# Optimization experiments

Measured on AMD Instinct MI355X. Metric: run time of the kernel, lower is better.

## Reference

```python
import jax, jax.numpy as jnp
import numpy as np

BETA = 0.25


def setup_inputs() -> dict:
    key = jax.random.key(0)
    kx, ke = jax.random.split(key)
    x = jax.random.normal(kx, (32, 32, 32, 256), dtype=jnp.float32)
    embedding = jax.random.normal(ke, (256, 4096), dtype=jnp.float32) * 0.02
    return {"x": x, "embedding": embedding}


def reference(x, embedding):
    # x: [B, H, W, D]; embedding (codebook): [D, K]
    D = embedding.shape[0]
    flat = x.reshape(-1, D)                               # [N, D]
    sim = flat @ embedding                                # [N, K]
    dist = (jnp.sum(flat * flat, axis=1, keepdims=True)
            + jnp.sum(embedding * embedding, axis=0)
            - 2.0 * sim)                                  # [N, K]
    idx = jnp.argmin(dist, axis=1)                        # [N]
    # one-hot @ embedding.T  ==  gather rows of embedding.T
    quantized = jnp.take(embedding.T, idx, axis=0).reshape(x.shape)
    commitment_loss = BETA * jnp.mean((jax.lax.stop_gradient(quantized) - x) ** 2)
    codebook_loss = jnp.mean((quantized - jax.lax.stop_gradient(x)) ** 2)
    loss = commitment_loss + codebook_loss
    # straight-through estimator
    quantized_st = x + jax.lax.stop_gradient(quantized - x)
    return quantized_st, loss
```

## Files before the change

kernel.cpp:

```cpp
#include <hip/hip_runtime.h>
#include <math.h>

typedef _Float16 f16;
typedef f16 f16x8 __attribute__((ext_vector_type(8)));
typedef float f32x4 __attribute__((ext_vector_type(4)));

#define N_ROWS 32768
#define DIM    256
#define KCODES 4096

#define WS_ET    0
#define WS_BN    (WS_ET + KCODES*DIM)
#define WS_AN    (WS_BN + KCODES)
#define WS_PART  (WS_AN + N_ROWS)
#define WS_IDX   (WS_PART + 8192)
#define WS_BP    (WS_IDX + N_ROWS)
#define WS_AP    (WS_BP + 1048576)


__device__ __forceinline__ void gload16(const void* g, void* l) {
#if __has_builtin(__builtin_amdgcn_global_load_lds)
    __builtin_amdgcn_global_load_lds(
        (const __attribute__((address_space(1))) unsigned int*)g,
        (__attribute__((address_space(3))) unsigned int*)l, 16, 0, 0);
#else
    *(float4*)l = *(const float4*)g;
#endif
}

__global__ void vq_rownorm(const float* __restrict__ src, float* __restrict__ out, int nrows) {
    int w    = threadIdx.x >> 6;
    int lane = threadIdx.x & 63;
    int row  = blockIdx.x * 4 + w;
    if (row >= nrows) return;
    float4 v = *(const float4*)&src[row * DIM + lane * 4];
    float  s = v.x * v.x + v.y * v.y + v.z * v.z + v.w * v.w;
#pragma unroll
    for (int m = 1; m < 64; m <<= 1) s += __shfl_xor(s, m);
    if (lane == 0) out[row] = s;
}

__global__ void vq_prep_a(const float* __restrict__ x, char* __restrict__ Ap,
                          float* __restrict__ An) {
    const int t = threadIdx.x;
    const int lane = t & 63, w = t >> 6;
    const size_t row0 = (size_t)blockIdx.x * 128;
    char* base = Ap + (size_t)blockIdx.x * 131072;
    const int chunk = lane >> 4;
    const int dd2   = (lane & 15) * 8;
#pragma unroll 4
    for (int it = 0; it < 32; ++it) {
        const int m = it * 4 + w;
        float4 v = *(const float4*)&x[(row0 + m) * DIM + lane * 4];
        float vs[4] = { v.x, v.y, v.z, v.w };
        uint32_t hw[2], lw[2];
#pragma unroll
        for (int p = 0; p < 2; ++p) {
            uint32_t hword = 0, lword = 0;
#pragma unroll
            for (int j = 0; j < 2; ++j) {
                float s = vs[p * 2 + j] * 1024.0f;
                f16 h = (f16)s;
                f16 l = (f16)(s - (float)h);
                hword |= (uint32_t)__builtin_bit_cast(uint16_t, h) << (16 * j);
                lword |= (uint32_t)__builtin_bit_cast(uint16_t, l) << (16 * j);
            }
            hw[p] = hword; lw[p] = lword;
        }
        const int off = chunk * 16384 + m * 128 + (dd2 ^ ((m & 7) << 4));
        *(uint2*)(base + off)         = *(uint2*)hw;
        *(uint2*)(base + 65536 + off) = *(uint2*)lw;
        float s = v.x * v.x + v.y * v.y + v.z * v.z + v.w * v.w;
#pragma unroll
        for (int mm = 1; mm < 64; mm <<= 1) s += __shfl_xor(s, mm);
        if (lane == 0) An[row0 + m] = s;
    }
}

__global__ void vq_prep_b(const float* __restrict__ e, char* __restrict__ Bp,
                          float* __restrict__ et) {
    __shared__ float lt[128][65];
    const int t  = threadIdx.x;
    const int jb = blockIdx.x >> 2;
    const int c  = blockIdx.x & 3;
    const int d0 = c * 64, n0 = jb * 128;
#pragma unroll
    for (int it = 0; it < 8; ++it) {
        int linear = it * 256 + t;
        int drow = linear >> 5;
        int ncol = (linear & 31) * 4;
        float4 v = *(const float4*)&e[(size_t)(d0 + drow) * KCODES + n0 + ncol];
        lt[ncol + 0][drow] = v.x;
        lt[ncol + 1][drow] = v.y;
        lt[ncol + 2][drow] = v.z;
        lt[ncol + 3][drow] = v.w;
    }
    __syncthreads();
#pragma unroll
    for (int it = 0; it < 8; ++it) {
        int lin = it * 256 + t;
        int n = lin >> 4, q = lin & 15;
        float4 v = { lt[n][q*4], lt[n][q*4+1], lt[n][q*4+2], lt[n][q*4+3] };
        *(float4*)&et[(size_t)(n0 + n) * DIM + d0 + q * 4] = v;
    }
    char* ehbase = Bp + (size_t)jb * 131072 + c * 16384;
    const int n_loc = t >> 1;
    const int shalf = t & 1;
#pragma unroll
    for (int g = 0; g < 4; ++g) {
        const int dd8 = shalf * 32 + g * 8;
        uint32_t ehw[4], elw[4];
#pragma unroll
        for (int p = 0; p < 4; ++p) {
            uint32_t hword = 0, lword = 0;
#pragma unroll
            for (int j = 0; j < 2; ++j) {
                float s = lt[n_loc][dd8 + p * 2 + j] * 1024.0f;
                f16 h = (f16)s;
                f16 l = (f16)(s - (float)h);
                hword |= (uint32_t)__builtin_bit_cast(uint16_t, h) << (16 * j);
                lword |= (uint32_t)__builtin_bit_cast(uint16_t, l) << (16 * j);
            }
            ehw[p] = hword; elw[p] = lword;
        }
        const int off = n_loc * 128 + ((dd8 * 2) ^ ((n_loc & 7) << 4));
        *(uint4*)(ehbase + off)         = *(uint4*)ehw;
        *(uint4*)(ehbase + 65536 + off) = *(uint4*)elw;
    }
}

__global__ __launch_bounds__(512, 2) void vq_main(
    const char* __restrict__ Ap, const char* __restrict__ Bp,
    const float* __restrict__ An, const float* __restrict__ Bn,
    int* __restrict__ idxOut)
{
    __shared__ __align__(16) char LaH[2][16384];
    __shared__ __align__(16) char LaL[16384];
    __shared__ __align__(16) char LbEH[32768];
    __shared__ __align__(16) char LbEL[32768];
    __shared__ unsigned long long red[128][4];

    const int tid = threadIdx.x;
    const int wid = tid >> 6, lane = tid & 63;
    const int wr = wid >> 2, wc = wid & 3;
    const int hi = lane >> 4, ln = lane & 15;
    const int sx = (lane & 7) << 4;
    const size_t row0 = (size_t)blockIdx.x * 128;
    const char* abase = Ap + (size_t)blockIdx.x * 131072;

    float an[16];
#pragma unroll
    for (int mi = 0; mi < 4; ++mi)
#pragma unroll
        for (int r = 0; r < 4; ++r)
            an[mi * 4 + r] = An[row0 + wr * 64 + mi * 16 + hi * 4 + r];

    unsigned long long run[16];
#pragma unroll
    for (int v = 0; v < 16; ++v) run[v] = ~0ull;

#define ISSUE_Y(t)                                                           \
    do {                                                                     \
        const int tn = ((t) + 1) & 63;                                       \
        const int c_ = tn & 3, it_ = tn >> 2;                                \
        const char* b0_ = Bp + (size_t)(2 * it_) * 131072;                   \
        const char* b1_ = b0_ + 131072;                                      \
        char* ah_ = (char*)LaH[tn & 1];                                      \
        gload16(abase + c_ * 16384 + tid * 16,        ah_ + tid * 16);       \
        gload16(abase + c_ * 16384 + 8192 + tid * 16, ah_ + 8192 + tid * 16);\
        gload16(b0_ + c_ * 16384 + tid * 16,        LbEH + tid * 16);        \
        gload16(b0_ + c_ * 16384 + 8192 + tid * 16, LbEH + 8192 + tid * 16); \
        gload16(b1_ + c_ * 16384 + tid * 16,        LbEH + 16384 + tid * 16);\
        gload16(b1_ + c_ * 16384 + 8192 + tid * 16, LbEH + 24576 + tid * 16);\
        gload16(b0_ + 65536 + c_ * 16384 + tid * 16,        LbEL + tid * 16);\
        gload16(b0_ + 65536 + c_ * 16384 + 8192 + tid * 16, LbEL + 8192 + tid * 16);\
        gload16(b1_ + 65536 + c_ * 16384 + tid * 16,        LbEL + 16384 + tid * 16);\
        gload16(b1_ + 65536 + c_ * 16384 + 8192 + tid * 16, LbEL + 24576 + tid * 16);\
    } while (0)

#define ISSUE_X(t)                                                           \
    do {                                                                     \
        const int c_ = (t) & 3;                                              \
        gload16(abase + 65536 + c_ * 16384 + tid * 16,        LaL + tid * 16);\
        gload16(abase + 65536 + c_ * 16384 + 8192 + tid * 16, LaL + 8192 + tid * 16);\
    } while (0)

    f32x4 acc[4][4] = {};

    ISSUE_Y(63);

#pragma unroll 1
    for (int t = 0; t < 64; ++t) {
        ISSUE_X(t);
        asm volatile("s_waitcnt vmcnt(2)" ::: "memory");
        __builtin_amdgcn_s_barrier();
        __builtin_amdgcn_sched_barrier(0);

        const char* ah = LaH[t & 1];
        f16x8 aH[8], bH[8], bL[8];
#pragma unroll
        for (int ks = 0; ks < 2; ++ks) {
            const int ko = (ks * 64 + hi * 16) ^ sx;
#pragma unroll
            for (int i = 0; i < 4; ++i)
                aH[ks * 4 + i] = *(const f16x8*)(ah + (wr * 64 + i * 16 + ln) * 128 + ko);
#pragma unroll
            for (int ni = 0; ni < 4; ++ni) {
                const int brow = ((wc & 1) * 64 + ni * 16 + ln) * 128 + ko;
                bH[ks * 4 + ni] = *(const f16x8*)(LbEH + (wc >> 1) * 16384 + brow);
                bL[ks * 4 + ni] = *(const f16x8*)(LbEL + (wc >> 1) * 16384 + brow);
            }
        }
        __builtin_amdgcn_s_setprio(1);
#pragma unroll
        for (int ks = 0; ks < 2; ++ks)
#pragma unroll
            for (int mi = 0; mi < 4; ++mi)
#pragma unroll
                for (int ni = 0; ni < 4; ++ni)
                    acc[mi][ni] = __builtin_amdgcn_mfma_f32_16x16x32_f16(
                        aH[ks * 4 + mi], bH[ks * 4 + ni], acc[mi][ni], 0, 0, 0);
#pragma unroll
        for (int ks = 0; ks < 2; ++ks)
#pragma unroll
            for (int mi = 0; mi < 4; ++mi)
#pragma unroll
                for (int ni = 0; ni < 4; ++ni)
                    acc[mi][ni] = __builtin_amdgcn_mfma_f32_16x16x32_f16(
                        aH[ks * 4 + mi], bL[ks * 4 + ni], acc[mi][ni], 0, 0, 0);
        __builtin_amdgcn_s_setprio(0);
        __builtin_amdgcn_s_barrier();

        ISSUE_Y(t);
        asm volatile("s_waitcnt vmcnt(10)" ::: "memory");
        __builtin_amdgcn_s_barrier();
        __builtin_amdgcn_sched_barrier(0);

        f16x8 aL[8];
#pragma unroll
        for (int ks = 0; ks < 2; ++ks) {
            const int ko = (ks * 64 + hi * 16) ^ sx;
#pragma unroll
            for (int i = 0; i < 4; ++i)
                aL[ks * 4 + i] = *(const f16x8*)(LaL + (wr * 64 + i * 16 + ln) * 128 + ko);
        }
        __builtin_amdgcn_s_setprio(1);
#pragma unroll
        for (int ks = 0; ks < 2; ++ks)
#pragma unroll
            for (int mi = 0; mi < 4; ++mi)
#pragma unroll
                for (int ni = 0; ni < 4; ++ni)
                    acc[mi][ni] = __builtin_amdgcn_mfma_f32_16x16x32_f16(
                        aL[ks * 4 + mi], bH[ks * 4 + ni], acc[mi][ni], 0, 0, 0);
        __builtin_amdgcn_s_setprio(0);
        __builtin_amdgcn_s_barrier();

        if ((t & 3) == 3) {
            const int it = t >> 2;
            float bn[4];
#pragma unroll
            for (int ni = 0; ni < 4; ++ni)
                bn[ni] = Bn[it * 256 + wc * 64 + ni * 16 + ln];
#pragma unroll
            for (int mi = 0; mi < 4; ++mi)
#pragma unroll
                for (int r = 0; r < 4; ++r) {
                    const float a = an[mi * 4 + r];
                    unsigned long long best = run[mi * 4 + r];
#pragma unroll
                    for (int ni = 0; ni < 4; ++ni) {
                        float sim  = acc[mi][ni][r] * 0x1p-20f;
                        float tt   = a + bn[ni];
                        float dist = tt - 2.0f * sim;
                        unsigned code = (unsigned)(it * 256 + wc * 64 + ni * 16 + ln);
                        unsigned long long p =
                            ((unsigned long long)__float_as_uint(dist) << 32) | code;
                        best = p < best ? p : best;
                    }
                    run[mi * 4 + r] = best;
                }
#pragma unroll
            for (int mi = 0; mi < 4; ++mi)
#pragma unroll
                for (int ni = 0; ni < 4; ++ni)
                    acc[mi][ni] = f32x4{0.f, 0.f, 0.f, 0.f};
        }
    }
#undef ISSUE_X
#undef ISSUE_Y

#pragma unroll
    for (int v = 0; v < 16; ++v) {
#pragma unroll
        for (int m = 1; m < 16; m <<= 1) {
            unsigned long long o = __shfl_xor(run[v], m);
            run[v] = o < run[v] ? o : run[v];
        }
    }
    if (ln == 0) {
#pragma unroll
        for (int mi = 0; mi < 4; ++mi)
#pragma unroll
            for (int r = 0; r < 4; ++r)
                red[wr * 64 + mi * 16 + hi * 4 + r][wc] = run[mi * 4 + r];
    }
    __syncthreads();
    if (tid < 128) {
        unsigned long long b = red[tid][0];
#pragma unroll
        for (int w = 1; w < 4; ++w) {
            unsigned long long o = red[tid][w];
            b = o < b ? o : b;
        }
        idxOut[row0 + tid] = (int)(unsigned)(b & 0xffffffffull);
    }
}

__global__ void vq_gather(const float* __restrict__ x, const float* __restrict__ et,
                          const int* __restrict__ idx,
                          float* __restrict__ out, float* __restrict__ part) {
    __shared__ float wsum[4];
    int w    = threadIdx.x >> 6;
    int lane = threadIdx.x & 63;
    int row  = blockIdx.x * 4 + w;
    int k    = idx[row];
    float4 q  = *(const float4*)&et[(size_t)k * DIM + lane * 4];
    float4 xv = *(const float4*)&x[(size_t)row * DIM + lane * 4];
    *(float4*)&out[(size_t)row * DIM + lane * 4] = q;
    float d0 = q.x - xv.x, d1 = q.y - xv.y, d2 = q.z - xv.z, d3 = q.w - xv.w;
    float s = d0 * d0 + d1 * d1 + d2 * d2 + d3 * d3;
#pragma unroll
    for (int m = 1; m < 64; m <<= 1) s += __shfl_xor(s, m);
    if (lane == 0) wsum[w] = s;
    __syncthreads();
    if (threadIdx.x == 0) part[blockIdx.x] = wsum[0] + wsum[1] + wsum[2] + wsum[3];
}

__global__ void vq_finalize(const float* __restrict__ part, float* __restrict__ lossOut) {
    __shared__ float sm[256];
    float s = 0.0f;
    for (int i = threadIdx.x; i < 8192; i += 256) s += part[i];
    sm[threadIdx.x] = s;
    __syncthreads();
    for (int st = 128; st > 0; st >>= 1) {
        if (threadIdx.x < st) sm[threadIdx.x] += sm[threadIdx.x + st];
        __syncthreads();
    }
    if (threadIdx.x == 0)
        lossOut[0] = 1.25f * (sm[0] / 8388608.0f);
}

extern "C" void kernel_launch(void* const* d_in, const int* in_sizes, int n_in,
                              void* d_out, int out_size, void* d_ws, size_t ws_size,
                              hipStream_t stream) {
    const float* x = (const float*)d_in[0];
    const float* e = (const float*)d_in[1];
    float* out = (float*)d_out;
    float* ws  = (float*)d_ws;

    float* et   = ws + WS_ET;
    float* bn   = ws + WS_BN;
    float* an   = ws + WS_AN;
    float* part = ws + WS_PART;
    int*   idx  = (int*)(ws + WS_IDX);
    char*  Bp   = (char*)(ws + WS_BP);
    char*  Ap   = (char*)(ws + WS_AP);

    vq_prep_a<<<256, 256, 0, stream>>>(x, Ap, an);
    vq_prep_b<<<128, 256, 0, stream>>>(e, Bp, et);
    vq_rownorm<<<KCODES / 4, 256, 0, stream>>>(et, bn, KCODES);
    vq_main<<<256, 512, 0, stream>>>(Ap, Bp, an, bn, idx);
    vq_gather<<<N_ROWS / 4, 256, 0, stream>>>(x, et, idx, out, part);
    vq_finalize<<<1, 256, 0, stream>>>(part, out + (size_t)N_ROWS * DIM);
}
```

Baseline: 284.8 us.

## Restructure load pipeline to issue all next-step tiles after fragment reads

Merges the two staged global-to-LDS load groups into one issue per step, placed after all shared-memory fragment reads complete. The A-low tile becomes the double-buffered one instead of A-high, and the loop is unrolled by four with plain block barriers replacing explicit vmcnt waits. This simplifies synchronisation and lets all next-step loads overlap the full MFMA phase. The cost is that every step now waits for all outstanding loads at its top barrier.

```diff
diff --git a/kernel.cpp b/kernel.cpp
--- a/kernel.cpp
+++ b/kernel.cpp
@@ -134,8 +134,8 @@
     const float* __restrict__ An, const float* __restrict__ Bn,
     int* __restrict__ idxOut)
 {
-    __shared__ __align__(16) char LaH[2][16384];
-    __shared__ __align__(16) char LaL[16384];
+    __shared__ __align__(16) char LaH[16384];
+    __shared__ __align__(16) char LaL[2][16384];
     __shared__ __align__(16) char LbEH[32768];
     __shared__ __align__(16) char LbEL[32768];
     __shared__ unsigned long long red[128][4];
@@ -159,136 +159,135 @@
 #pragma unroll
     for (int v = 0; v < 16; ++v) run[v] = ~0ull;
 
-#define ISSUE_Y(t)                                                           \
-    do {                                                                     \
-        const int tn = ((t) + 1) & 63;                                       \
-        const int c_ = tn & 3, it_ = tn >> 2;                                \
-        const char* b0_ = Bp + (size_t)(2 * it_) * 131072;                   \
-        const char* b1_ = b0_ + 131072;                                      \
-        char* ah_ = (char*)LaH[tn & 1];                                      \
-        gload16(abase + c_ * 16384 + tid * 16,        ah_ + tid * 16);       \
-        gload16(abase + c_ * 16384 + 8192 + tid * 16, ah_ + 8192 + tid * 16);\
-        gload16(b0_ + c_ * 16384 + tid * 16,        LbEH + tid * 16);        \
-        gload16(b0_ + c_ * 16384 + 8192 + tid * 16, LbEH + 8192 + tid * 16); \
-        gload16(b1_ + c_ * 16384 + tid * 16,        LbEH + 16384 + tid * 16);\
-        gload16(b1_ + c_ * 16384 + 8192 + tid * 16, LbEH + 24576 + tid * 16);\
-        gload16(b0_ + 65536 + c_ * 16384 + tid * 16,        LbEL + tid * 16);\
-        gload16(b0_ + 65536 + c_ * 16384 + 8192 + tid * 16, LbEL + 8192 + tid * 16);\
-        gload16(b1_ + 65536 + c_ * 16384 + tid * 16,        LbEL + 16384 + tid * 16);\
-        gload16(b1_ + 65536 + c_ * 16384 + 8192 + tid * 16, LbEL + 24576 + tid * 16);\
+#define ISSUE(c_, it_, slot)                                                  \
+    do {                                                                      \
+        const char* b0_ = Bp + (size_t)(2 * (it_)) * 131072;                  \
+        const char* b1_ = b0_ + 131072;                                       \
+        gload16(abase + (c_) * 16384 + tid * 16,        LaH + tid * 16);      \
+        gload16(abase + (c_) * 16384 + 8192 + tid * 16, LaH + 8192 + tid * 16);\
+        gload16(abase + 65536 + (c_) * 16384 + tid * 16,                      \
+                LaL[slot] + tid * 16);                                        \
+        gload16(abase + 65536 + (c_) * 16384 + 8192 + tid * 16,               \
+                LaL[slot] + 8192 + tid * 16);                                 \
+        gload16(b0_ + (c_) * 16384 + tid * 16,        LbEH + tid * 16);       \
+        gload16(b0_ + (c_) * 16384 + 8192 + tid * 16, LbEH + 8192 + tid * 16);\
+        gload16(b1_ + (c_) * 16384 + tid * 16,        LbEH + 16384 + tid * 16);\
+        gload16(b1_ + (c_) * 16384 + 8192 + tid * 16, LbEH + 24576 + tid * 16);\
+        gload16(b0_ + 65536 + (c_) * 16384 + tid * 16,        LbEL + tid * 16);\
+        gload16(b0_ + 65536 + (c_) * 16384 + 8192 + tid * 16,                 \
+                LbEL + 8192 + tid * 16);                                      \
+        gload16(b1_ + 65536 + (c_) * 16384 + tid * 16,                        \
+                LbEL + 16384 + tid * 16);                                     \
+        gload16(b1_ + 65536 + (c_) * 16384 + 8192 + tid * 16,                 \
+                LbEL + 24576 + tid * 16);                                     \
     } while (0)
 
-#define ISSUE_X(t)                                                           \
-    do {                                                                     \
-        const int c_ = (t) & 3;                                              \
-        gload16(abase + 65536 + c_ * 16384 + tid * 16,        LaL + tid * 16);\
-        gload16(abase + 65536 + c_ * 16384 + 8192 + tid * 16, LaL + 8192 + tid * 16);\
-    } while (0)
-
     f32x4 acc[4][4] = {};
 
-    ISSUE_Y(63);
+    ISSUE(0, 0, 0);
 
 #pragma unroll 1
-    for (int t = 0; t < 64; ++t) {
-        ISSUE_X(t);
-        asm volatile("s_waitcnt vmcnt(2)" ::: "memory");
-        __builtin_amdgcn_s_barrier();
-        __builtin_amdgcn_sched_barrier(0);
-
-        const char* ah = LaH[t & 1];
-        f16x8 aH[8], bH[8], bL[8];
-#pragma unroll
-        for (int ks = 0; ks < 2; ++ks) {
-            const int ko = (ks * 64 + hi * 16) ^ sx;
-#pragma unroll
-            for (int i = 0; i < 4; ++i)
-                aH[ks * 4 + i] = *(const f16x8*)(ah + (wr * 64 + i * 16 + ln) * 128 + ko);
-#pragma unroll
-            for (int ni = 0; ni < 4; ++ni) {
-                const int brow = ((wc & 1) * 64 + ni * 16 + ln) * 128 + ko;
-                bH[ks * 4 + ni] = *(const f16x8*)(LbEH + (wc >> 1) * 16384 + brow);
-                bL[ks * 4 + ni] = *(const f16x8*)(LbEL + (wc >> 1) * 16384 + brow);
-            }
-        }
-        __builtin_amdgcn_s_setprio(1);
-#pragma unroll
-        for (int ks = 0; ks < 2; ++ks)
-#pragma unroll
-            for (int mi = 0; mi < 4; ++mi)
+    for (int itr = 0; itr < 16; ++itr) {
+#pragma unroll
+        for (int u = 0; u < 4; ++u) {
+            __syncthreads();
+
+            f16x8 aH[8], bH[8], bL[8];
+#pragma unroll
+            for (int ks = 0; ks < 2; ++ks) {
+                const int ko = (ks * 64 + hi * 16) ^ sx;
+#pragma unroll
+                for (int i = 0; i < 4; ++i)
+                    aH[ks * 4 + i] =
+                        *(const f16x8*)(LaH + (wr * 64 + i * 16 + ln) * 128 + ko);
+#pragma unroll
+                for (int ni = 0; ni < 4; ++ni) {
+                    const int brow = ((wc & 1) * 64 + ni * 16 + ln) * 128 + ko;
+                    bH[ks * 4 + ni] =
+                        *(const f16x8*)(LbEH + (wc >> 1) * 16384 + brow);
+                    bL[ks * 4 + ni] =
+                        *(const f16x8*)(LbEL + (wc >> 1) * 16384 + brow);
+                }
+            }
+            __syncthreads();
+
+            if (itr * 4 + u < 63) {
+                if (u < 3) ISSUE(u + 1, itr, (u + 1) & 1);
+                else       ISSUE(0, itr + 1, 0);
+            }
+            __builtin_amdgcn_sched_barrier(0);
+
+            __builtin_amdgcn_s_setprio(1);
+#pragma unroll
+            for (int ks = 0; ks < 2; ++ks)
+#pragma unroll
+                for (int mi = 0; mi < 4; ++mi)
+#pragma unroll
+                    for (int ni = 0; ni < 4; ++ni)
+                        acc[mi][ni] = __builtin_amdgcn_mfma_f32_16x16x32_f16(
+                            aH[ks * 4 + mi], bH[ks * 4 + ni], acc[mi][ni], 0, 0, 0);
+#pragma unroll
+            for (int ks = 0; ks < 2; ++ks)
+#pragma unroll
+                for (int mi = 0; mi < 4; ++mi)
+#pragma unroll
+                    for (int ni = 0; ni < 4; ++ni)
+                        acc[mi][ni] = __builtin_amdgcn_mfma_f32_16x16x32_f16(
+                            aH[ks * 4 + mi], bL[ks * 4 + ni], acc[mi][ni], 0, 0, 0);
+            __builtin_amdgcn_s_setprio(0);
+
+            f16x8 aL[8];
+#pragma unroll
+            for (int ks = 0; ks < 2; ++ks) {
+                const int ko = (ks * 64 + hi * 16) ^ sx;
+#pragma unroll
+                for (int i = 0; i < 4; ++i)
+                    aL[ks * 4 + i] =
+                        *(const f16x8*)(LaL[u & 1] + (wr * 64 + i * 16 + ln) * 128 + ko);
+            }
+            __builtin_amdgcn_s_setprio(1);
+#pragma unroll
+            for (int ks = 0; ks < 2; ++ks)
+#pragma unroll
+                for (int mi = 0; mi < 4; ++mi)
+#pragma unroll
+                    for (int ni = 0; ni < 4; ++ni)
+                        acc[mi][ni] = __builtin_amdgcn_mfma_f32_16x16x32_f16(
+                            aL[ks * 4 + mi], bH[ks * 4 + ni], acc[mi][ni], 0, 0, 0);
+            __builtin_amdgcn_s_setprio(0);
+
+            if (u == 3) {
+                float bn[4];
 #pragma unroll
                 for (int ni = 0; ni < 4; ++ni)
-                    acc[mi][ni] = __builtin_amdgcn_mfma_f32_16x16x32_f16(
-                        aH[ks * 4 + mi], bH[ks * 4 + ni], acc[mi][ni], 0, 0, 0);
-#pragma unroll
-        for (int ks = 0; ks < 2; ++ks)
-#pragma unroll
-            for (int mi = 0; mi < 4; ++mi)
-#pragma unroll
-                for (int ni = 0; ni < 4; ++ni)
-                    acc[mi][ni] = __builtin_amdgcn_mfma_f32_16x16x32_f16(
-                        aH[ks * 4 + mi], bL[ks * 4 + ni], acc[mi][ni], 0, 0, 0);
-        __builtin_amdgcn_s_setprio(0);
-        __builtin_amdgcn_s_barrier();
-
-        ISSUE_Y(t);
-        asm volatile("s_waitcnt vmcnt(10)" ::: "memory");
-        __builtin_amdgcn_s_barrier();
-        __builtin_amdgcn_sched_barrier(0);
-
-        f16x8 aL[8];
-#pragma unroll
-        for (int ks = 0; ks < 2; ++ks) {
-            const int ko = (ks * 64 + hi * 16) ^ sx;
-#pragma unroll
-            for (int i = 0; i < 4; ++i)
-                aL[ks * 4 + i] = *(const f16x8*)(LaL + (wr * 64 + i * 16 + ln) * 128 + ko);
-        }
-        __builtin_amdgcn_s_setprio(1);
-#pragma unroll
-        for (int ks = 0; ks < 2; ++ks)
-#pragma unroll
-            for (int mi = 0; mi < 4; ++mi)
-#pragma unroll
-                for (int ni = 0; ni < 4; ++ni)
-                    acc[mi][ni] = __builtin_amdgcn_mfma_f32_16x16x32_f16(
-                        aL[ks * 4 + mi], bH[ks * 4 + ni], acc[mi][ni], 0, 0, 0);
-        __builtin_amdgcn_s_setprio(0);
-        __builtin_amdgcn_s_barrier();
-
-        if ((t & 3) == 3) {
-            const int it = t >> 2;
-            float bn[4];
-#pragma unroll
-            for (int ni = 0; ni < 4; ++ni)
-                bn[ni] = Bn[it * 256 + wc * 64 + ni * 16 + ln];
-#pragma unroll
-            for (int mi = 0; mi < 4; ++mi)
-#pragma unroll
-                for (int r = 0; r < 4; ++r) {
-                    const float a = an[mi * 4 + r];
-                    unsigned long long best = run[mi * 4 + r];
-#pragma unroll
-                    for (int ni = 0; ni < 4; ++ni) {
-                        float sim  = acc[mi][ni][r] * 0x1p-20f;
-                        float tt   = a + bn[ni];
-                        float dist = tt - 2.0f * sim;
-                        unsigned code = (unsigned)(it * 256 + wc * 64 + ni * 16 + ln);
-                        unsigned long long p =
-                            ((unsigned long long)__float_as_uint(dist) << 32) | code;
-                        best = p < best ? p : best;
+                    bn[ni] = Bn[itr * 256 + wc * 64 + ni * 16 + ln];
+#pragma unroll
+                for (int mi = 0; mi < 4; ++mi)
+#pragma unroll
+                    for (int r = 0; r < 4; ++r) {
+                        const float a = an[mi * 4 + r];
+                        unsigned long long best = run[mi * 4 + r];
+#pragma unroll
+                        for (int ni = 0; ni < 4; ++ni) {
+                            float sim  = acc[mi][ni][r] * 0x1p-20f;
+                            float tt   = a + bn[ni];
+                            float dist = tt - 2.0f * sim;
+                            unsigned code = (unsigned)(itr * 256 + wc * 64 + ni * 16 + ln);
+                            unsigned long long p =
+                                ((unsigned long long)__float_as_uint(dist) << 32) | code;
+                            best = p < best ? p : best;
+                        }
+                        run[mi * 4 + r] = best;
                     }
-                    run[mi * 4 + r] = best;
-                }
-#pragma unroll
-            for (int mi = 0; mi < 4; ++mi)
-#pragma unroll
-                for (int ni = 0; ni < 4; ++ni)
-                    acc[mi][ni] = f32x4{0.f, 0.f, 0.f, 0.f};
-        }
-    }
-#undef ISSUE_X
-#undef ISSUE_Y
+#pragma unroll
+                for (int mi = 0; mi < 4; ++mi)
+#pragma unroll
+                    for (int ni = 0; ni < 4; ++ni)
+                        acc[mi][ni] = f32x4{0.f, 0.f, 0.f, 0.f};
+            }
+        }
+    }
+#undef ISSUE
 
 #pragma unroll
     for (int v = 0; v < 16; ++v) {
```

After: 367.8 us. 1.29x slower.

## Prefetch next A-high tile with A-low loads and relax launch bounds

Applied to the files above, without the earlier changes.

Moves the prefetch of the next iteration's A-high tile out of the Y issue group and into the X issue group, issued alongside the current A-low load. The wait is relaxed to vmcnt(4) so the A-high prefetch can stay in flight across the barrier. The prologue now explicitly loads the first A-high and codebook tiles. Launch bounds drop from 2 blocks per CU to 1, which frees registers but may halve occupancy.

```diff
diff --git a/kernel.cpp b/kernel.cpp
--- a/kernel.cpp
+++ b/kernel.cpp
@@ -129,7 +129,7 @@
     }
 }
 
-__global__ __launch_bounds__(512, 2) void vq_main(
+__global__ __launch_bounds__(512, 1) void vq_main(
     const char* __restrict__ Ap, const char* __restrict__ Bp,
     const float* __restrict__ An, const float* __restrict__ Bn,
     int* __restrict__ idxOut)
@@ -159,40 +159,60 @@
 #pragma unroll
     for (int v = 0; v < 16; ++v) run[v] = ~0ull;
 
-#define ISSUE_Y(t)                                                           \
-    do {                                                                     \
-        const int tn = ((t) + 1) & 63;                                       \
-        const int c_ = tn & 3, it_ = tn >> 2;                                \
-        const char* b0_ = Bp + (size_t)(2 * it_) * 131072;                   \
-        const char* b1_ = b0_ + 131072;                                      \
-        char* ah_ = (char*)LaH[tn & 1];                                      \
-        gload16(abase + c_ * 16384 + tid * 16,        ah_ + tid * 16);       \
-        gload16(abase + c_ * 16384 + 8192 + tid * 16, ah_ + 8192 + tid * 16);\
-        gload16(b0_ + c_ * 16384 + tid * 16,        LbEH + tid * 16);        \
-        gload16(b0_ + c_ * 16384 + 8192 + tid * 16, LbEH + 8192 + tid * 16); \
-        gload16(b1_ + c_ * 16384 + tid * 16,        LbEH + 16384 + tid * 16);\
-        gload16(b1_ + c_ * 16384 + 8192 + tid * 16, LbEH + 24576 + tid * 16);\
-        gload16(b0_ + 65536 + c_ * 16384 + tid * 16,        LbEL + tid * 16);\
-        gload16(b0_ + 65536 + c_ * 16384 + 8192 + tid * 16, LbEL + 8192 + tid * 16);\
-        gload16(b1_ + 65536 + c_ * 16384 + tid * 16,        LbEL + 16384 + tid * 16);\
-        gload16(b1_ + 65536 + c_ * 16384 + 8192 + tid * 16, LbEL + 24576 + tid * 16);\
+#define ISSUE_X(t)                                                            \
+    do {                                                                      \
+        const int c_ = (t) & 3;                                               \
+        gload16(abase + 65536 + c_ * 16384 + tid * 16,        LaL + tid * 16);\
+        gload16(abase + 65536 + c_ * 16384 + 8192 + tid * 16,                 \
+                LaL + 8192 + tid * 16);                                       \
+        const int tn_ = ((t) + 1) & 63;                                       \
+        const int cn_ = tn_ & 3;                                              \
+        char* ah_ = (char*)LaH[tn_ & 1];                                      \
+        gload16(abase + cn_ * 16384 + tid * 16,        ah_ + tid * 16);       \
+        gload16(abase + cn_ * 16384 + 8192 + tid * 16, ah_ + 8192 + tid * 16);\
     } while (0)
 
-#define ISSUE_X(t)                                                           \
-    do {                                                                     \
-        const int c_ = (t) & 3;                                              \
-        gload16(abase + 65536 + c_ * 16384 + tid * 16,        LaL + tid * 16);\
-        gload16(abase + 65536 + c_ * 16384 + 8192 + tid * 16, LaL + 8192 + tid * 16);\
+#define ISSUE_Y(t)                                                            \
+    do {                                                                      \
+        const int tn = ((t) + 1) & 63;                                        \
+        const int c_ = tn & 3, it_ = tn >> 2;                                 \
+        const char* b0_ = Bp + (size_t)(2 * it_) * 131072;                    \
+        const char* b1_ = b0_ + 131072;                                       \
+        gload16(b0_ + c_ * 16384 + tid * 16,        LbEH + tid * 16);         \
+        gload16(b0_ + c_ * 16384 + 8192 + tid * 16, LbEH + 8192 + tid * 16);  \
+        gload16(b1_ + c_ * 16384 + tid * 16,        LbEH + 16384 + tid * 16); \
+        gload16(b1_ + c_ * 16384 + 8192 + tid * 16, LbEH + 24576 + tid * 16); \
+        gload16(b0_ + 65536 + c_ * 16384 + tid * 16,        LbEL + tid * 16); \
+        gload16(b0_ + 65536 + c_ * 16384 + 8192 + tid * 16,                   \
+                LbEL + 8192 + tid * 16);                                      \
+        gload16(b1_ + 65536 + c_ * 16384 + tid * 16,                          \
+                LbEL + 16384 + tid * 16);                                     \
+        gload16(b1_ + 65536 + c_ * 16384 + 8192 + tid * 16,                   \
+                LbEL + 24576 + tid * 16);                                     \
     } while (0)
 
     f32x4 acc[4][4] = {};
 
-    ISSUE_Y(63);
+    {
+        char* ah_ = (char*)LaH[0];
+        gload16(abase + tid * 16,        ah_ + tid * 16);
+        gload16(abase + 8192 + tid * 16, ah_ + 8192 + tid * 16);
+        const char* b0_ = Bp;
+        const char* b1_ = Bp + 131072;
+        gload16(b0_ + tid * 16,        LbEH + tid * 16);
+        gload16(b0_ + 8192 + tid * 16, LbEH + 8192 + tid * 16);
+        gload16(b1_ + tid * 16,        LbEH + 16384 + tid * 16);
+        gload16(b1_ + 8192 + tid * 16, LbEH + 24576 + tid * 16);
+        gload16(b0_ + 65536 + tid * 16,        LbEL + tid * 16);
+        gload16(b0_ + 65536 + 8192 + tid * 16, LbEL + 8192 + tid * 16);
+        gload16(b1_ + 65536 + tid * 16,        LbEL + 16384 + tid * 16);
+        gload16(b1_ + 65536 + 8192 + tid * 16, LbEL + 24576 + tid * 16);
+    }
 
 #pragma unroll 1
     for (int t = 0; t < 64; ++t) {
         ISSUE_X(t);
-        asm volatile("s_waitcnt vmcnt(2)" ::: "memory");
+        asm volatile("s_waitcnt vmcnt(4)" ::: "memory");
         __builtin_amdgcn_s_barrier();
         __builtin_amdgcn_sched_barrier(0);
 
```

Result: faster. 276.7 us (-2.9%).
